# Performance work log

Measured on AMD Instinct MI355X. Metric: run time of the kernel, lower is better.

Reference implementation:

```python
import jax, jax.numpy as jnp
import numpy as np

C = 1024        # number of classes
N = 8           # proxies per class
ALLNUM = C * N  # 8192 total proxies
DIM = 512
R = 0.05
TOPK = int(np.ceil(R * ALLNUM))  # 410
LAM = 0.3
B = 2048


def setup_inputs() -> dict:
    key = jax.random.key(0)
    k1, k2, k3 = jax.random.split(key, 3)
    inp = jax.random.normal(k1, (B, DIM), dtype=jnp.float32)
    target = jax.random.randint(k2, (B,), 0, C, dtype=jnp.int64)
    # kaiming-uniform-initialized proxies approximated by scaled normal init
    proxies = jax.random.normal(k3, (DIM, ALLNUM), dtype=jnp.float32)
    instance_label = jnp.repeat(jnp.arange(C, dtype=jnp.int64), N)  # [ALLNUM]
    return {"input": inp, "target": target, "Proxies": proxies,
            "instance_label": instance_label}


def reference(input, target, Proxies, instance_label):
    # L2-normalize each proxy column (F.normalize along dim=0, eps=1e-12)
    norm = jnp.maximum(jnp.linalg.norm(Proxies, axis=0, keepdims=True), 1e-12)
    centers = Proxies / norm                             # [DIM, ALLNUM]
    similarity = input @ centers                          # [B, ALLNUM]

    positive_mask = (target[:, None] == instance_label[None, :]).astype(similarity.dtype)
    _, indices = jax.lax.top_k(similarity + 1000.0 * positive_mask, TOPK)  # [B, TOPK]

    rows = jnp.arange(similarity.shape[0])[:, None]
    mask = jnp.zeros_like(similarity).at[rows, indices].set(1.0)
    prob_a = mask * similarity                            # sparse-masked similarities

    y_instance_onehot = jax.nn.one_hot(instance_label, C, dtype=similarity.dtype)  # [ALLNUM, C]
    logits = prob_a @ y_instance_onehot                   # [B, C]

    y_target_onehot = jax.nn.one_hot(target, C, dtype=similarity.dtype)  # [B, C]
    logits_mask = 1.0 - (logits == 0.0).astype(similarity.dtype)

    # scale_mask_softmax with scale=1 along dim=1
    e = jnp.exp(logits) * logits_mask
    predict = e / (1e-8 + jnp.sum(e, axis=1, keepdims=True))
    lossClassify = jnp.mean(jnp.sum(-y_target_onehot * jnp.log(predict + 1e-20), axis=1))

    # proxy regularizer: cross-entropy of proxy-vs-class logits
    simCenter = centers.T @ centers                       # [ALLNUM, ALLNUM]
    centers_logits = simCenter @ y_instance_onehot        # [ALLNUM, C]
    logp = jax.nn.log_softmax(centers_logits, axis=1)
    reg = -jnp.mean(jnp.take_along_axis(logp, instance_label[:, None], axis=1))

    return (lossClassify + LAM * reg, lossClassify)
```

## Files before the change

### kernel.cpp

```cpp
#include <hip/hip_runtime.h>
#include <hip/hip_bf16.h>
#include <math.h>

#define C_CLS   1024
#define NPROXY  8
#define ALLNUM  8192
#define DIM     512
#define TOPK    410
#define LAM     0.3f
#define BATCH   2048

typedef __bf16 bf16x8 __attribute__((ext_vector_type(8)));
typedef float floatx4 __attribute__((ext_vector_type(4)));
typedef unsigned short ushort_t;

#define WS_RNORM 0
#define WS_SIG   8192
#define WS_LP    10240
#define WS_RP    12288
#define WS_ABF   14336
#define WS_PBF   538624
#define WS_STBF  2635776
#define WS_LOG   2897920
#define WS_SIM   7092224

__device__ inline float block_reduce(float v, int is_max, float* red, int t) {
    #pragma unroll
    for (int o = 32; o > 0; o >>= 1) {
        float w = __shfl_down(v, o);
        v = is_max ? fmaxf(v, w) : (v + w);
    }
    __syncthreads();
    if ((t & 63) == 0) red[t >> 6] = v;
    __syncthreads();
    return is_max ? fmaxf(fmaxf(red[0], red[1]), fmaxf(red[2], red[3]))
                  : (red[0] + red[1] + red[2] + red[3]);
}

__device__ inline ushort_t f2bf(float f) {
    unsigned u = __float_as_uint(f);
    return (ushort_t)((u + 0x7FFFu + ((u >> 16) & 1u)) >> 16);
}

__device__ inline void ld_g2l_16(const void* g, void* l) {
    __builtin_amdgcn_global_load_lds(
        (const __attribute__((address_space(1))) unsigned int*)g,
        (__attribute__((address_space(3))) unsigned int*)l,
        16, 0, 0);
}

__device__ inline unsigned f2ord(float f) {
    unsigned u = __float_as_uint(f);
    return (u & 0x80000000u) ? ~u : (u | 0x80000000u);
}

__global__ __launch_bounds__(256) void k_prep1(const float* __restrict__ P,
                                               const float* __restrict__ input,
                                               float* __restrict__ rnorm,
                                               float* __restrict__ rowsig,
                                               ushort_t* __restrict__ Abf,
                                               ushort_t* __restrict__ Pbf) {
    __shared__ float tile[32][33];
    float* cred = &tile[0][0];
    int bx = blockIdx.x, t = threadIdx.x;
    if (bx < 256) {
        int tc = t & 31, g = t >> 5;
        int c = bx * 32 + tc;
        const float* pc = P + (size_t)(g * 64) * ALLNUM + c;
        float s = 0.f;
        #pragma unroll 8
        for (int d = 0; d < 64; ++d) {
            float v = pc[(size_t)d * ALLNUM];
            s += v * v;
        }
        cred[g * 32 + tc] = s;
        __syncthreads();
        if (g == 0) {
            float tot = 0.f;
            #pragma unroll
            for (int k = 0; k < 8; ++k) tot += cred[k * 32 + tc];
            rnorm[c] = 1.0f / fmaxf(sqrtf(tot), 1e-12f);
        }
    } else if (bx < 256 + 1024) {
        int a = bx - 256;
        int idx = a * 256 + t;
        float4 v = ((const float4*)input)[idx];
        ushort4 o;
        o.x = f2bf(v.x); o.y = f2bf(v.y); o.z = f2bf(v.z); o.w = f2bf(v.w);
        ((ushort4*)Abf)[idx] = o;
        float sq = v.x * v.x + v.y * v.y + v.z * v.z + v.w * v.w;
        #pragma unroll
        for (int off = 32; off > 0; off >>= 1) sq += __shfl_down(sq, off);
        int lane = t & 63, w = t >> 6;
        if (lane == 0) cred[w] = sq;
        __syncthreads();
        if (t == 0) {
            rowsig[2 * a]     = sqrtf(cred[0] + cred[1]);
            rowsig[2 * a + 1] = sqrtf(cred[2] + cred[3]);
        }
    } else {
        int id = bx - 1280;
        int c0 = (id & 255) * 32, r0 = (id >> 8) * 32;
        int tc = t & 31, tr = t >> 5;
        #pragma unroll
        for (int p = 0; p < 4; ++p)
            tile[tr + p * 8][tc] = P[(size_t)(r0 + tr + p * 8) * ALLNUM + c0 + tc];
        __syncthreads();
        #pragma unroll
        for (int p = 0; p < 4; ++p) {
            int oc = tr + p * 8;
            Pbf[(size_t)(c0 + oc) * DIM + r0 + tc] = f2bf(tile[tc][oc]);
        }
    }
}

__global__ __launch_bounds__(256) void k_stage2(const ushort_t* __restrict__ A,
                                                const ushort_t* __restrict__ B,
                                                const float* __restrict__ P,
                                                const float* __restrict__ rnorm,
                                                float* __restrict__ sim,
                                                ushort_t* __restrict__ Stbf) {
    __shared__ __align__(16) ushort_t smem[2 * 128 * 64];
    int bx = blockIdx.x, t = threadIdx.x;

    if (bx < 1024) {
        ushort_t* sA = smem;
        ushort_t* sB = smem + 128 * 64;
        int w = t >> 6, lane = t & 63;
        int wm = w >> 1, wn = w & 1;
        int bj = (bx & 63) * 128, bi = (bx >> 6) * 128;

        floatx4 acc[4][4];
        #pragma unroll
        for (int tm = 0; tm < 4; ++tm)
            #pragma unroll
            for (int tn = 0; tn < 4; ++tn)
                acc[tm][tn] = (floatx4){0.f, 0.f, 0.f, 0.f};

        for (int k0 = 0; k0 < DIM; k0 += 64) {
            #pragma unroll
            for (int it = 0; it < 4; ++it) {
                int c = w * 256 + it * 64 + lane;
                int m = c >> 3, s = c & 7;
                int q = s ^ (m & 7);
                ld_g2l_16(A + ((size_t)(bi + m) << 9) + k0 + q * 8,
                          &sA[(w * 256 + it * 64) * 8]);
            }
            #pragma unroll
            for (int it = 0; it < 4; ++it) {
                int c = w * 256 + it * 64 + lane;
                int m = c >> 3, s = c & 7;
                int q = s ^ (m & 7);
                ld_g2l_16(B + ((size_t)(bj + m) << 9) + k0 + q * 8,
                          &sB[(w * 256 + it * 64) * 8]);
            }
            asm volatile("s_waitcnt vmcnt(0)" ::: "memory");
            __syncthreads();

            #pragma unroll
            for (int kk = 0; kk < 2; ++kk) {
                bf16x8 af[4], bfr[4];
                int ml = lane & 15, q = lane >> 4;
                #pragma unroll
                for (int tm = 0; tm < 4; ++tm) {
                    int m = wm * 64 + tm * 16 + ml;
                    int s = (kk * 4 + q) ^ (m & 7);
                    af[tm] = *(const bf16x8*)&sA[m * 64 + s * 8];
                }
                #pragma unroll
                for (int tn = 0; tn < 4; ++tn) {
                    int n = wn * 64 + tn * 16 + ml;
                    int s = (kk * 4 + q) ^ (n & 7);
                    bfr[tn] = *(const bf16x8*)&sB[n * 64 + s * 8];
                }
                #pragma unroll
                for (int tm = 0; tm < 4; ++tm)
                    #pragma unroll
                    for (int tn = 0; tn < 4; ++tn)
                        acc[tm][tn] = __builtin_amdgcn_mfma_f32_16x16x32_bf16(
                            af[tm], bfr[tn], acc[tm][tn], 0, 0, 0);
            }
            __syncthreads();
        }

        int ml = lane & 15, qd = lane >> 4;
        #pragma unroll
        for (int tm = 0; tm < 4; ++tm) {
            int rowb = bi + wm * 64 + tm * 16 + qd * 4;
            #pragma unroll
            for (int tn = 0; tn < 4; ++tn) {
                int col = bj + wn * 64 + tn * 16 + ml;
                float sc = rnorm[col];
                #pragma unroll
                for (int i = 0; i < 4; ++i)
                    sim[(size_t)(rowb + i) * ALLNUM + col] = acc[tm][tn][i] * sc;
            }
        }
    } else {
        float* tile = (float*)smem;
        int id = bx - 1024;
        int c0 = (id & 31) * 32, d0 = (id >> 5) * 32;
        int cl = t & 31, dl8 = t >> 5;
        #pragma unroll
        for (int p = 0; p < 4; ++p) {
            int d = d0 + dl8 + 8 * p;
            int c = c0 + cl;
            const float* pp = P + (size_t)d * ALLNUM + c * NPROXY;
            const float* rn = rnorm + c * NPROXY;
            float4 a = *(const float4*)pp;
            float4 b = *(const float4*)(pp + 4);
            float4 ra = *(const float4*)rn;
            float4 rb = *(const float4*)(rn + 4);
            tile[(dl8 + 8 * p) * 33 + cl] =
                a.x * ra.x + a.y * ra.y + a.z * ra.z + a.w * ra.w +
                b.x * rb.x + b.y * rb.y + b.z * rb.z + b.w * rb.w;
        }
        __syncthreads();
        #pragma unroll
        for (int p = 0; p < 4; ++p) {
            int cl2 = dl8 + 8 * p, dl2 = t & 31;
            Stbf[(size_t)(c0 + cl2) * DIM + d0 + dl2] = f2bf(tile[dl2 * 33 + cl2]);
        }
    }
}

#define SEL_CAP 1024
#define GCAP    64

__device__ inline void suffix_select1(unsigned* s_hist, unsigned kk,
                                      unsigned* s_wtot, unsigned* sh_bin,
                                      unsigned* sh_k, int t, int lane, int wid) {
    unsigned h = s_hist[t];
    unsigned v = h;
    #pragma unroll
    for (int off = 1; off < 64; off <<= 1) {
        unsigned o = __shfl_down(v, off);
        if (lane + off < 64) v += o;
    }
    if (lane == 0) s_wtot[wid] = v;
    __syncthreads();
    unsigned above = v - h;
    for (int w2 = wid + 1; w2 < 4; ++w2) above += s_wtot[w2];
    unsigned cum = above + h;
    if (cum >= kk && above < kk) { *sh_bin = (unsigned)t; *sh_k = kk - above; }
    __syncthreads();
}

__global__ __launch_bounds__(256) void k_stage3(const float* __restrict__ sim,
                                                const int* __restrict__ target,
                                                const float* __restrict__ rowsig,
                                                float* __restrict__ loss_part,
                                                const ushort_t* __restrict__ Pbf,
                                                const ushort_t* __restrict__ Stbf,
                                                const float* __restrict__ rnorm,
                                                ushort_t* __restrict__ logits) {
    __shared__ __align__(16) unsigned char smem[16384];
    int bx = blockIdx.x, t = threadIdx.x;
    int lane = t & 63, wid = t >> 6;

    if (bx < 2048) {
        float*    s_cls  = (float*)smem;
        float*    s_bval = (float*)(smem + 4096);
        ushort_t* s_bcol = (ushort_t*)(smem + 8192);
        unsigned* s_bhist= (unsigned*)(smem + 10240);
        float*    s_gval = (float*)(smem + 11264);
        unsigned* s_wtot = (unsigned*)(smem + 11520);
        unsigned* shv    = (unsigned*)(smem + 11536);
        float*    shf    = (float*)(smem + 11552);
        int*      shi    = (int*)(smem + 11556);
        float*    red    = (float*)(smem + 11568);

        int b = bx;
        const float* row = sim + (size_t)b * ALLNUM;
        int tgt = target[b];
        float sig = rowsig[b] * (1.0f / 22.616f);
        float hiT = 1.80f * sig, loT = 1.47f * sig;
        float binscale = 256.0f / (hiT - loT);

        float4 v4[8];
        #pragma unroll
        for (int p = 0; p < 8; ++p) v4[p] = ((const float4*)row)[t + 256 * p];

        if (t == 0) { shv[0] = 0; shv[1] = 0; }
        s_bhist[t] = 0;
        #pragma unroll
        for (int i = 0; i < 4; ++i) s_cls[t + 256 * i] = 0.f;
        __syncthreads();

        float ndef = 0.f;
        #pragma unroll
        for (int p = 0; p < 8; ++p) {
            int f = t + 256 * p;
            int cls = f >> 1;
            const float* pv = (const float*)&v4[p];
            if (cls == tgt) {
                atomicAdd(&s_cls[tgt], pv[0] + pv[1] + pv[2] + pv[3]);
            } else {
                float ds = 0.f;
                #pragma unroll
                for (int e = 0; e < 4; ++e) {
                    float v = pv[e];
                    if (v >= hiT) { ds += v; ndef += 1.f; }
                    else if (v >= loT) {
                        unsigned idx = atomicAdd(&shv[0], 1u);
                        if (idx < SEL_CAP) { s_bval[idx] = v; s_bcol[idx] = (ushort_t)(4 * f + e); }
                        int bin = (int)((v - loT) * binscale);
                        bin = (bin > 255) ? 255 : bin;
                        atomicAdd(&s_bhist[bin], 1u);
                    }
                }
                float o = __shfl_xor(ds, 1);
                float s2 = ds + o;
                if ((t & 1) == 0 && s2 != 0.f) atomicAdd(&s_cls[cls], s2);
            }
        }
        float ndefT = block_reduce(ndef, 0, red, t);
        int bc = (int)shv[0];
        int kq = (TOPK - NPROXY) - (int)ndefT;
        if (t == 0) shi[0] = (kq < 0 || bc < kq || bc > SEL_CAP) ? 1 : 0;
        __syncthreads();

        if (!shi[0]) {
            if (kq > 0) {
                suffix_select1(s_bhist, (unsigned)kq, s_wtot, &shv[2], &shv[3], t, lane, wid);
                int B = (int)shv[2];
                int knew = (int)shv[3];
                for (int j = t; j < bc; j += 256) {
                    float v = s_bval[j];
                    int bin = (int)((v - loT) * binscale);
                    bin = (bin > 255) ? 255 : bin;
                    if (bin == B) {
                        unsigned g = atomicAdd(&shv[1], 1u);
                        if (g < GCAP) s_gval[g] = v;
                    }
                }
                __syncthreads();
                int gc = (int)shv[1];
                if (gc <= GCAP) {
                    if (t < gc) {
                        float vj = s_gval[t];
                        unsigned g = 0, geq = 0;
                        for (int i = 0; i < gc; ++i) {
                            float vi = s_gval[i];
                            g   += (vi > vj) ? 1u : 0u;
                            geq += (vi >= vj) ? 1u : 0u;
                        }
                        if (g < (unsigned)knew && geq >= (unsigned)knew) shf[0] = vj;
                    }
                } else {
                    for (int j = t; j < bc; j += 256) {
                        float vj = s_bval[j];
                        unsigned g = 0, geq = 0;
                        for (int i = 0; i < bc; ++i) {
                            float vi = s_bval[i];
                            g   += (vi > vj) ? 1u : 0u;
                            geq += (vi >= vj) ? 1u : 0u;
                        }
                        if (g < (unsigned)kq && geq >= (unsigned)kq) shf[0] = vj;
                    }
                }
                __syncthreads();
                float thr = shf[0];
                for (int j = t; j < bc; j += 256)
                    if (s_bval[j] >= thr)
                        atomicAdd(&s_cls[s_bcol[j] >> 3], s_bval[j]);
            }
        } else {
            __syncthreads();
            #pragma unroll
            for (int i = 0; i < 4; ++i) s_cls[t + 256 * i] = 0.f;
            __syncthreads();
            #pragma unroll
            for (int p = 0; p < 8; ++p) {
                int f = t + 256 * p;
                const float* pv = (const float*)&v4[p];
                if ((f >> 1) == tgt)
                    atomicAdd(&s_cls[tgt], pv[0] + pv[1] + pv[2] + pv[3]);
            }
            unsigned L = 0u, R = 0xFFFFFFFFu;
            for (int it = 0; it < 33 && R - L > 1; ++it) {
                unsigned mid = L + ((R - L) >> 1);
                float c = 0.f;
                #pragma unroll
                for (int p = 0; p < 8; ++p) {
                    int f = t + 256 * p;
                    const float* pv = (const float*)&v4[p];
                    if ((f >> 1) != tgt) {
                        #pragma unroll
                        for (int e = 0; e < 4; ++e)
                            c += (f2ord(pv[e]) >= mid) ? 1.f : 0.f;
                    }
                }
                c = block_reduce(c, 0, red, t);
                if (c >= (float)(TOPK - NPROXY)) L = mid; else R = mid;
                __syncthreads();
            }
            #pragma unroll
            for (int p = 0; p < 8; ++p) {
                int f = t + 256 * p;
                const float* pv = (const float*)&v4[p];
                if ((f >> 1) != tgt) {
                    #pragma unroll
                    for (int e = 0; e < 4; ++e)
                        if (f2ord(pv[e]) >= L)
                            atomicAdd(&s_cls[f >> 1], pv[e]);
                }
            }
        }
        __syncthreads();

        float4 cv = ((const float4*)s_cls)[t];
        float m = -1e30f;
        if (cv.x != 0.0f) m = fmaxf(m, cv.x);
        if (cv.y != 0.0f) m = fmaxf(m, cv.y);
        if (cv.z != 0.0f) m = fmaxf(m, cv.z);
        if (cv.w != 0.0f) m = fmaxf(m, cv.w);
        m = block_reduce(m, 1, red, t);
        float se = 0.f;
        if (cv.x != 0.0f) se += expf(cv.x - m);
        if (cv.y != 0.0f) se += expf(cv.y - m);
        if (cv.z != 0.0f) se += expf(cv.z - m);
        if (cv.w != 0.0f) se += expf(cv.w - m);
        se = block_reduce(se, 0, red, t);
        if (t == 0) {
            float lt = s_cls[tgt];
            float predict_t = expf(lt - m) / (1e-8f * expf(-m) + se);
            loss_part[b] = -logf(predict_t + 1e-20f);
        }
    } else {
        ushort_t* sA = (ushort_t*)smem;
        ushort_t* sB = (ushort_t*)(smem + 8192);
        int id = bx - 2048;
        int bj = (id & 15) * 64;
        int bi = (id >> 4) * 64;
        int w = wid;
        int wm = w >> 1, wn = w & 1;

        floatx4 acc[2][2];
        #pragma unroll
        for (int tm = 0; tm < 2; ++tm)
            #pragma unroll
            for (int tn = 0; tn < 2; ++tn)
                acc[tm][tn] = (floatx4){0.f, 0.f, 0.f, 0.f};

        for (int k0 = 0; k0 < DIM; k0 += 64) {
            #pragma unroll
            for (int it = 0; it < 2; ++it) {
                int c = (w * 2 + it) * 64 + lane;
                int m = c >> 3, s = c & 7;
                int q = s ^ (m & 7);
                ld_g2l_16(Pbf + ((size_t)(bi + m) << 9) + k0 + q * 8,
                          &sA[((w * 2 + it) * 64) * 8]);
            }
            #pragma unroll
            for (int it = 0; it < 2; ++it) {
                int c = (w * 2 + it) * 64 + lane;
                int m = c >> 3, s = c & 7;
                int q = s ^ (m & 7);
                ld_g2l_16(Stbf + ((size_t)(bj + m) << 9) + k0 + q * 8,
                          &sB[((w * 2 + it) * 64) * 8]);
            }
            asm volatile("s_waitcnt vmcnt(0)" ::: "memory");
            __syncthreads();

            #pragma unroll
            for (int kk = 0; kk < 2; ++kk) {
                bf16x8 af[2], bfr[2];
                int ml = lane & 15, q = lane >> 4;
                #pragma unroll
                for (int tm = 0; tm < 2; ++tm) {
                    int m = wm * 32 + tm * 16 + ml;
                    int s = (kk * 4 + q) ^ (m & 7);
                    af[tm] = *(const bf16x8*)&sA[m * 64 + s * 8];
                }
                #pragma unroll
                for (int tn = 0; tn < 2; ++tn) {
                    int n = wn * 32 + tn * 16 + ml;
                    int s = (kk * 4 + q) ^ (n & 7);
                    bfr[tn] = *(const bf16x8*)&sB[n * 64 + s * 8];
                }
                #pragma unroll
                for (int tm = 0; tm < 2; ++tm)
                    #pragma unroll
                    for (int tn = 0; tn < 2; ++tn)
                        acc[tm][tn] = __builtin_amdgcn_mfma_f32_16x16x32_bf16(
                            af[tm], bfr[tn], acc[tm][tn], 0, 0, 0);
            }
            __syncthreads();
        }

        int ml = lane & 15, qd = lane >> 4;
        #pragma unroll
        for (int tm = 0; tm < 2; ++tm) {
            int rowb = bi + wm * 32 + tm * 16 + qd * 4;
            float4 rnr = *(const float4*)&rnorm[rowb];
            #pragma unroll
            for (int tn = 0; tn < 2; ++tn) {
                int col = bj + wn * 32 + tn * 16 + ml;
                #pragma unroll
                for (int i = 0; i < 4; ++i)
                    logits[(size_t)(rowb + i) * C_CLS + col] =
                        f2bf(acc[tm][tn][i] * ((const float*)&rnr)[i]);
            }
        }
    }
}

__global__ __launch_bounds__(256) void k_regloss(const ushort_t* __restrict__ logits,
                                                 float* __restrict__ reg_part) {
    __shared__ float bsum[4];
    int t = threadIdx.x, lane = t & 63, wid = t >> 6;
    int i = blockIdx.x * 4 + wid;
    const ushort_t* row = logits + (size_t)i * C_CLS;
    uint4 c0 = ((const uint4*)row)[lane];
    uint4 c1 = ((const uint4*)(row + 512))[lane];

    float f[16];
    const unsigned* u0 = (const unsigned*)&c0;
    const unsigned* u1 = (const unsigned*)&c1;
    #pragma unroll
    for (int k = 0; k < 4; ++k) {
        f[2 * k]     = __uint_as_float(u0[k] << 16);
        f[2 * k + 1] = __uint_as_float(u0[k] & 0xFFFF0000u);
        f[8 + 2 * k]     = __uint_as_float(u1[k] << 16);
        f[8 + 2 * k + 1] = __uint_as_float(u1[k] & 0xFFFF0000u);
    }

    int cstar = i >> 3;
    int chunk = cstar >> 9, within = cstar & 511;
    float sd = 0.f;
    if (lane == (within >> 3)) sd = f[chunk * 8 + (within & 7)];

    float m = -1e30f;
    #pragma unroll
    for (int k = 0; k < 16; ++k) m = fmaxf(m, f[k]);
    #pragma unroll
    for (int off = 32; off > 0; off >>= 1) m = fmaxf(m, __shfl_xor(m, off));

    float se = 0.f;
    #pragma unroll
    for (int k = 0; k < 16; ++k) se += expf(f[k] - m);
    #pragma unroll
    for (int off = 32; off > 0; off >>= 1) se += __shfl_xor(se, off);
    #pragma unroll
    for (int off = 32; off > 0; off >>= 1) sd += __shfl_xor(sd, off);

    if (lane == 0) bsum[wid] = m + logf(se) - sd;
    __syncthreads();
    if (t == 0)
        reg_part[blockIdx.x] = bsum[0] + bsum[1] + bsum[2] + bsum[3];
}

__global__ __launch_bounds__(256) void k_final(const float* __restrict__ lp,
                                               const float* __restrict__ rp,
                                               float* __restrict__ out) {
    __shared__ float red[4];
    int t = threadIdx.x;
    float4 a = ((const float4*)lp)[t];
    float4 b = ((const float4*)lp)[t + 256];
    float4 c = ((const float4*)rp)[t];
    float4 d = ((const float4*)rp)[t + 256];
    float ls = a.x + a.y + a.z + a.w + b.x + b.y + b.z + b.w;
    float rs = c.x + c.y + c.z + c.w + d.x + d.y + d.z + d.w;
    ls = block_reduce(ls, 0, red, t);
    rs = block_reduce(rs, 0, red, t);
    if (t == 0) {
        float lc = ls / (float)BATCH;
        float rg = rs / (float)ALLNUM;
        out[0] = lc + LAM * rg;
        out[1] = lc;
    }
}

extern "C" void kernel_launch(void* const* d_in, const int* in_sizes, int n_in,
                              void* d_out, int out_size, void* d_ws, size_t ws_size,
                              hipStream_t stream) {
    const float* input  = (const float*)d_in[0];
    const int*   target = (const int*)d_in[1];
    const float* P      = (const float*)d_in[2];

    float* ws       = (float*)d_ws;
    float* rnorm    = ws + WS_RNORM;
    float* rowsig   = ws + WS_SIG;
    float* loss_part= ws + WS_LP;
    float* reg_part = ws + WS_RP;
    ushort_t* Abf   = (ushort_t*)(ws + WS_ABF);
    ushort_t* Pbf   = (ushort_t*)(ws + WS_PBF);
    ushort_t* Stbf  = (ushort_t*)(ws + WS_STBF);
    ushort_t* logits= (ushort_t*)(ws + WS_LOG);
    float* sim      = ws + WS_SIM;
    float* out      = (float*)d_out;

    hipLaunchKernelGGL(k_prep1, dim3(256 + 1024 + 4096), dim3(256), 0, stream,
                       P, input, rnorm, rowsig, Abf, Pbf);
    hipLaunchKernelGGL(k_stage2, dim3(1024 + 512), dim3(256), 0, stream,
                       Abf, Pbf, P, rnorm, sim, Stbf);
    hipLaunchKernelGGL(k_stage3, dim3(2048 + 2048), dim3(256), 0, stream,
                       sim, target, rowsig, loss_part, Pbf, Stbf, rnorm, logits);
    hipLaunchKernelGGL(k_regloss, dim3(ALLNUM / 4), dim3(256), 0, stream,
                       logits, reg_part);
    hipLaunchKernelGGL(k_final, dim3(1), dim3(256), 0, stream,
                       loss_part, reg_part, out);
}
```

Baseline: 153.8 us.

## Store similarity in bf16 and fuse regularizer softmax into GEMM epilogue

The similarity matrix is now written as bf16 instead of fp32, which halves the traffic between the GEMM and the top-k stage, and each thread now owns a whole class of 8 proxies so the shared-memory atomics go away. The proxy-vs-class logits are no longer written out. The GEMM epilogue instead accumulates the row sums of exp without max subtraction, adds them to a per-row buffer with atomics, and records the diagonal term. This removes the k_regloss kernel and the logits buffer. The costs are bf16 rounding of similarities, which can change the top-k ties, and an unstabilized exp sum that relies on the cosine logits being bounded.

```diff
diff --git a/kernel.cpp b/kernel.cpp
--- a/kernel.cpp
+++ b/kernel.cpp
@@ -17,12 +17,12 @@
 #define WS_RNORM 0
 #define WS_SIG   8192
 #define WS_LP    10240
-#define WS_RP    12288
-#define WS_ABF   14336
-#define WS_PBF   538624
-#define WS_STBF  2635776
-#define WS_LOG   2897920
-#define WS_SIM   7092224
+#define WS_RSE   12288
+#define WS_DIAG  20480
+#define WS_ABF   28672
+#define WS_PBF   552960
+#define WS_STBF  2650112
+#define WS_SIMBF 2912256
 
 __device__ inline float block_reduce(float v, int is_max, float* red, int t) {
     #pragma unroll
@@ -58,6 +58,7 @@
                                                const float* __restrict__ input,
                                                float* __restrict__ rnorm,
                                                float* __restrict__ rowsig,
+                                               float* __restrict__ rse,
                                                ushort_t* __restrict__ Abf,
                                                ushort_t* __restrict__ Pbf) {
     __shared__ float tile[32][33];
@@ -74,6 +75,8 @@
             s += v * v;
         }
         cred[g * 32 + tc] = s;
+        int gid = bx * 256 + t;
+        if (gid < 8192) rse[gid] = 0.f;
         __syncthreads();
         if (g == 0) {
             float tot = 0.f;
@@ -118,7 +121,7 @@
                                                 const ushort_t* __restrict__ B,
                                                 const float* __restrict__ P,
                                                 const float* __restrict__ rnorm,
-                                                float* __restrict__ sim,
+                                                ushort_t* __restrict__ simbf,
                                                 ushort_t* __restrict__ Stbf) {
     __shared__ __align__(16) ushort_t smem[2 * 128 * 64];
     int bx = blockIdx.x, t = threadIdx.x;
@@ -193,7 +196,7 @@
                 float sc = rnorm[col];
                 #pragma unroll
                 for (int i = 0; i < 4; ++i)
-                    sim[(size_t)(rowb + i) * ALLNUM + col] = acc[tm][tn][i] * sc;
+                    simbf[(size_t)(rowb + i) * ALLNUM + col] = f2bf(acc[tm][tn][i] * sc);
             }
         }
     } else {
@@ -246,14 +249,15 @@
     __syncthreads();
 }
 
-__global__ __launch_bounds__(256) void k_stage3(const float* __restrict__ sim,
+__global__ __launch_bounds__(256) void k_stage3(const ushort_t* __restrict__ simbf,
                                                 const int* __restrict__ target,
                                                 const float* __restrict__ rowsig,
                                                 float* __restrict__ loss_part,
                                                 const ushort_t* __restrict__ Pbf,
                                                 const ushort_t* __restrict__ Stbf,
                                                 const float* __restrict__ rnorm,
-                                                ushort_t* __restrict__ logits) {
+                                                float* __restrict__ rse,
+                                                float* __restrict__ diag) {
     __shared__ __align__(16) unsigned char smem[16384];
     int bx = blockIdx.x, t = threadIdx.x;
     int lane = t & 63, wid = t >> 6;
@@ -271,47 +275,53 @@
         float*    red    = (float*)(smem + 11568);
 
         int b = bx;
-        const float* row = sim + (size_t)b * ALLNUM;
+        const ushort_t* row = simbf + (size_t)b * ALLNUM;
         int tgt = target[b];
         float sig = rowsig[b] * (1.0f / 22.616f);
         float hiT = 1.80f * sig, loT = 1.47f * sig;
         float binscale = 256.0f / (hiT - loT);
 
-        float4 v4[8];
-        #pragma unroll
-        for (int p = 0; p < 8; ++p) v4[p] = ((const float4*)row)[t + 256 * p];
+        uint4 r4[4];
+        #pragma unroll
+        for (int p = 0; p < 4; ++p) r4[p] = ((const uint4*)row)[t + 256 * p];
+        float f[4][8];
+        #pragma unroll
+        for (int p = 0; p < 4; ++p) {
+            const unsigned* u = (const unsigned*)&r4[p];
+            #pragma unroll
+            for (int k = 0; k < 4; ++k) {
+                f[p][2 * k]     = __uint_as_float(u[k] << 16);
+                f[p][2 * k + 1] = __uint_as_float(u[k] & 0xFFFF0000u);
+            }
+        }
 
         if (t == 0) { shv[0] = 0; shv[1] = 0; }
         s_bhist[t] = 0;
-        #pragma unroll
-        for (int i = 0; i < 4; ++i) s_cls[t + 256 * i] = 0.f;
         __syncthreads();
 
         float ndef = 0.f;
         #pragma unroll
-        for (int p = 0; p < 8; ++p) {
-            int f = t + 256 * p;
-            int cls = f >> 1;
-            const float* pv = (const float*)&v4[p];
+        for (int p = 0; p < 4; ++p) {
+            int cls = t + 256 * p;
             if (cls == tgt) {
-                atomicAdd(&s_cls[tgt], pv[0] + pv[1] + pv[2] + pv[3]);
+                float s8 = f[p][0] + f[p][1] + f[p][2] + f[p][3] +
+                           f[p][4] + f[p][5] + f[p][6] + f[p][7];
+                s_cls[cls] = s8;
             } else {
                 float ds = 0.f;
                 #pragma unroll
-                for (int e = 0; e < 4; ++e) {
-                    float v = pv[e];
+                for (int e = 0; e < 8; ++e) {
+                    float v = f[p][e];
                     if (v >= hiT) { ds += v; ndef += 1.f; }
                     else if (v >= loT) {
                         unsigned idx = atomicAdd(&shv[0], 1u);
-                        if (idx < SEL_CAP) { s_bval[idx] = v; s_bcol[idx] = (ushort_t)(4 * f + e); }
+                        if (idx < SEL_CAP) { s_bval[idx] = v; s_bcol[idx] = (ushort_t)(cls * 8 + e); }
                         int bin = (int)((v - loT) * binscale);
                         bin = (bin > 255) ? 255 : bin;
                         atomicAdd(&s_bhist[bin], 1u);
                     }
                 }
-                float o = __shfl_xor(ds, 1);
-                float s2 = ds + o;
-                if ((t & 1) == 0 && s2 != 0.f) atomicAdd(&s_cls[cls], s2);
+                s_cls[cls] = ds;
             }
         }
         float ndefT = block_reduce(ndef, 0, red, t);
@@ -366,29 +376,17 @@
                         atomicAdd(&s_cls[s_bcol[j] >> 3], s_bval[j]);
             }
         } else {
-            __syncthreads();
-            #pragma unroll
-            for (int i = 0; i < 4; ++i) s_cls[t + 256 * i] = 0.f;
-            __syncthreads();
-            #pragma unroll
-            for (int p = 0; p < 8; ++p) {
-                int f = t + 256 * p;
-                const float* pv = (const float*)&v4[p];
-                if ((f >> 1) == tgt)
-                    atomicAdd(&s_cls[tgt], pv[0] + pv[1] + pv[2] + pv[3]);
-            }
             unsigned L = 0u, R = 0xFFFFFFFFu;
             for (int it = 0; it < 33 && R - L > 1; ++it) {
                 unsigned mid = L + ((R - L) >> 1);
                 float c = 0.f;
                 #pragma unroll
-                for (int p = 0; p < 8; ++p) {
-                    int f = t + 256 * p;
-                    const float* pv = (const float*)&v4[p];
-                    if ((f >> 1) != tgt) {
+                for (int p = 0; p < 4; ++p) {
+                    int cls = t + 256 * p;
+                    if (cls != tgt) {
                         #pragma unroll
-                        for (int e = 0; e < 4; ++e)
-                            c += (f2ord(pv[e]) >= mid) ? 1.f : 0.f;
+                        for (int e = 0; e < 8; ++e)
+                            c += (f2ord(f[p][e]) >= mid) ? 1.f : 0.f;
                     }
                 }
                 c = block_reduce(c, 0, red, t);
@@ -396,14 +394,14 @@
                 __syncthreads();
             }
             #pragma unroll
-            for (int p = 0; p < 8; ++p) {
-                int f = t + 256 * p;
-                const float* pv = (const float*)&v4[p];
-                if ((f >> 1) != tgt) {
+            for (int p = 0; p < 4; ++p) {
+                int cls = t + 256 * p;
+                if (cls != tgt) {
+                    float s = 0.f;
                     #pragma unroll
-                    for (int e = 0; e < 4; ++e)
-                        if (f2ord(pv[e]) >= L)
-                            atomicAdd(&s_cls[f >> 1], pv[e]);
+                    for (int e = 0; e < 8; ++e)
+                        if (f2ord(f[p][e]) >= L) s += f[p][e];
+                    s_cls[cls] = s;
                 }
             }
         }
@@ -495,73 +493,38 @@
             int rowb = bi + wm * 32 + tm * 16 + qd * 4;
             float4 rnr = *(const float4*)&rnorm[rowb];
             #pragma unroll
-            for (int tn = 0; tn < 2; ++tn) {
-                int col = bj + wn * 32 + tn * 16 + ml;
-                #pragma unroll
-                for (int i = 0; i < 4; ++i)
-                    logits[(size_t)(rowb + i) * C_CLS + col] =
-                        f2bf(acc[tm][tn][i] * ((const float*)&rnr)[i]);
+            for (int i = 0; i < 4; ++i) {
+                int rowg = rowb + i;
+                float rn = ((const float*)&rnr)[i];
+                float esum = 0.f;
+                #pragma unroll
+                for (int tn = 0; tn < 2; ++tn) {
+                    int colg = bj + wn * 32 + tn * 16 + ml;
+                    float v = acc[tm][tn][i] * rn;
+                    esum += expf(v);
+                    if (colg == (rowg >> 3)) diag[rowg] = v;
+                }
+                #pragma unroll
+                for (int off = 1; off < 16; off <<= 1)
+                    esum += __shfl_xor(esum, off);
+                if (ml == 0) atomicAdd(&rse[rowg], esum);
             }
         }
     }
 }
 
-__global__ __launch_bounds__(256) void k_regloss(const ushort_t* __restrict__ logits,
-                                                 float* __restrict__ reg_part) {
-    __shared__ float bsum[4];
-    int t = threadIdx.x, lane = t & 63, wid = t >> 6;
-    int i = blockIdx.x * 4 + wid;
-    const ushort_t* row = logits + (size_t)i * C_CLS;
-    uint4 c0 = ((const uint4*)row)[lane];
-    uint4 c1 = ((const uint4*)(row + 512))[lane];
-
-    float f[16];
-    const unsigned* u0 = (const unsigned*)&c0;
-    const unsigned* u1 = (const unsigned*)&c1;
-    #pragma unroll
-    for (int k = 0; k < 4; ++k) {
-        f[2 * k]     = __uint_as_float(u0[k] << 16);
-        f[2 * k + 1] = __uint_as_float(u0[k] & 0xFFFF0000u);
-        f[8 + 2 * k]     = __uint_as_float(u1[k] << 16);
-        f[8 + 2 * k + 1] = __uint_as_float(u1[k] & 0xFFFF0000u);
-    }
-
-    int cstar = i >> 3;
-    int chunk = cstar >> 9, within = cstar & 511;
-    float sd = 0.f;
-    if (lane == (within >> 3)) sd = f[chunk * 8 + (within & 7)];
-
-    float m = -1e30f;
-    #pragma unroll
-    for (int k = 0; k < 16; ++k) m = fmaxf(m, f[k]);
-    #pragma unroll
-    for (int off = 32; off > 0; off >>= 1) m = fmaxf(m, __shfl_xor(m, off));
-
-    float se = 0.f;
-    #pragma unroll
-    for (int k = 0; k < 16; ++k) se += expf(f[k] - m);
-    #pragma unroll
-    for (int off = 32; off > 0; off >>= 1) se += __shfl_xor(se, off);
-    #pragma unroll
-    for (int off = 32; off > 0; off >>= 1) sd += __shfl_xor(sd, off);
-
-    if (lane == 0) bsum[wid] = m + logf(se) - sd;
-    __syncthreads();
-    if (t == 0)
-        reg_part[blockIdx.x] = bsum[0] + bsum[1] + bsum[2] + bsum[3];
-}
-
 __global__ __launch_bounds__(256) void k_final(const float* __restrict__ lp,
-                                               const float* __restrict__ rp,
+                                               const float* __restrict__ rse,
+                                               const float* __restrict__ diag,
                                                float* __restrict__ out) {
     __shared__ float red[4];
     int t = threadIdx.x;
     float4 a = ((const float4*)lp)[t];
     float4 b = ((const float4*)lp)[t + 256];
-    float4 c = ((const float4*)rp)[t];
-    float4 d = ((const float4*)rp)[t + 256];
     float ls = a.x + a.y + a.z + a.w + b.x + b.y + b.z + b.w;
-    float rs = c.x + c.y + c.z + c.w + d.x + d.y + d.z + d.w;
+    float rs = 0.f;
+    for (int r = t; r < ALLNUM; r += 256)
+        rs += logf(rse[r]) - diag[r];
     ls = block_reduce(ls, 0, red, t);
     rs = block_reduce(rs, 0, red, t);
     if (t == 0) {
@@ -583,22 +546,20 @@
     float* rnorm    = ws + WS_RNORM;
     float* rowsig   = ws + WS_SIG;
     float* loss_part= ws + WS_LP;
-    float* reg_part = ws + WS_RP;
+    float* rse      = ws + WS_RSE;
+    float* diag     = ws + WS_DIAG;
     ushort_t* Abf   = (ushort_t*)(ws + WS_ABF);
     ushort_t* Pbf   = (ushort_t*)(ws + WS_PBF);
     ushort_t* Stbf  = (ushort_t*)(ws + WS_STBF);
-    ushort_t* logits= (ushort_t*)(ws + WS_LOG);
-    float* sim      = ws + WS_SIM;
+    ushort_t* simbf = (ushort_t*)(ws + WS_SIMBF);
     float* out      = (float*)d_out;
 
     hipLaunchKernelGGL(k_prep1, dim3(256 + 1024 + 4096), dim3(256), 0, stream,
-                       P, input, rnorm, rowsig, Abf, Pbf);
+                       P, input, rnorm, rowsig, rse, Abf, Pbf);
     hipLaunchKernelGGL(k_stage2, dim3(1024 + 512), dim3(256), 0, stream,
-                       Abf, Pbf, P, rnorm, sim, Stbf);
+                       Abf, Pbf, P, rnorm, simbf, Stbf);
     hipLaunchKernelGGL(k_stage3, dim3(2048 + 2048), dim3(256), 0, stream,
-                       sim, target, rowsig, loss_part, Pbf, Stbf, rnorm, logits);
-    hipLaunchKernelGGL(k_regloss, dim3(ALLNUM / 4), dim3(256), 0, stream,
-                       logits, reg_part);
+                       simbf, target, rowsig, loss_part, Pbf, Stbf, rnorm, rse, diag);
     hipLaunchKernelGGL(k_final, dim3(1), dim3(256), 0, stream,
-                       loss_part, reg_part, out);
-}
+                       loss_part, rse, diag, out);
+}
```

Result: slower. 158.7 us (+3.2%).
